# Performance work log

Hardware: AMD Instinct MI355X
Metric: run time of the kernel (lower is better)

## Reference

```python
import jax, jax.numpy as jnp
import numpy as np

K = 4                 # max_block_size (depthwise conv kernel size)
BLOCKS = (1, 2, 3, 4) # block sizes, offset 0
DS = 4                # downsample_factor
BLOCK_MULT = 12       # lcm(1,2,3,4)
DIM = 512
NUM_TOKENS = 256


def setup_inputs() -> dict:
    key = jax.random.key(0)
    ks = jax.random.split(key, 8)
    b, n = 4, 4096
    s = 0.02
    return {
        "x": jax.random.randint(ks[0], (b, n), 0, NUM_TOKENS),
        "emb": jax.random.normal(ks[1], (NUM_TOKENS, DIM), dtype=jnp.float32) * s,
        "conv_w": jax.random.normal(ks[2], (DIM, K), dtype=jnp.float32) * s,   # depthwise Conv1d weight [d,1,K] squeezed
        "conv_b": jax.random.normal(ks[3], (DIM,), dtype=jnp.float32) * s,
        "proj_w": jax.random.normal(ks[4], (DIM, DIM), dtype=jnp.float32) * s,  # 1x1 conv == linear [out,in]
        "proj_b": jax.random.normal(ks[5], (DIM,), dtype=jnp.float32) * s,
        "score_w": jax.random.normal(ks[6], (DIM,), dtype=jnp.float32) * s,     # nn.Linear(dim,1)
        "score_b": jax.random.normal(ks[7], (), dtype=jnp.float32) * s,
    }


def reference(x, emb, conv_w, conv_b, proj_w, proj_b, score_w, score_b):
    b, n = x.shape
    h = emb[x]  # [b, n, d] token embedding (gather)

    # pos_conv: pad (K-1) at sequence end, depthwise conv (valid), then pointwise proj
    hp = jnp.pad(h, ((0, 0), (0, K - 1), (0, 0)))
    y = conv_b + sum(hp[:, k:k + n, :] * conv_w[:, k] for k in range(K))  # [b, n, d]
    h = y @ proj_w.T + proj_b

    # pad sequence to multiple of lcm of block sizes
    L = -(-n // BLOCK_MULT) * BLOCK_MULT
    h = jnp.pad(h, ((0, 0), (0, L - n), (0, 0)))

    # multi-scale block mean pooling, upsampled back to length L
    reprs = []
    for bs in BLOCKS:
        r = h.reshape(b, L // bs, bs, DIM).mean(axis=2)     # [b, L/bs, d]
        reprs.append(jnp.repeat(r, bs, axis=1))             # [b, L, d]
    block_reprs = jnp.stack(reprs, axis=2)                  # [b, L, nb, d]

    # per-position block scores
    scores = block_reprs @ score_w + score_b                # [b, L, nb]
    scores = jax.nn.softmax(scores, axis=2)

    # consensus attention over positions (d = nb = len(BLOCKS))
    sim = jnp.einsum('bid,bjd->bij', scores, scores)        # [b, L, L]
    attn = jax.nn.softmax(sim, axis=-1)
    scores = jnp.einsum('bij,bjm->bim', attn, scores)       # [b, L, nb]

    # fuse block representations and downsample
    out = jnp.einsum('bnkd,bnk->bnd', block_reprs, scores)  # [b, L, d]
    m = -(-n // DS) * DS                                    # == n (4096 divisible by 4)
    out = out[:, :m].reshape(b, m // DS, DS, DIM).mean(axis=2)
    return out
```

## Files before the change

kernel.cpp:

```cpp
#include <hip/hip_runtime.h>
#include <hip/hip_bf16.h>

#define B_ 4
#define N_ 4096
#define L_ 4104
#define D_ 512
#define RT 17
#define JC2 32
#define CH2 129
#define BK 64

typedef __attribute__((ext_vector_type(8))) short bf16x8;
typedef __attribute__((ext_vector_type(4))) float f32x4;

__device__ __forceinline__ float bf2f(unsigned short u) {
  union { unsigned u; float f; } c; c.u = ((unsigned)u) << 16; return c.f;
}

__global__ __launch_bounds__(256) void k_g(const float* __restrict__ emb,
    const float* __restrict__ pw, const float* __restrict__ cwp,
    const float* __restrict__ cb, const float* __restrict__ pb,
    float* __restrict__ G, float* __restrict__ biasp) {
  __shared__ __align__(16) __hip_bfloat16 As[2][64 * BK];
  __shared__ __align__(16) __hip_bfloat16 Bs[2][128 * BK];
  __shared__ __align__(16) float cwS[512];
  __shared__ float red[4];
  const int bx = blockIdx.x;
  const int t = threadIdx.x;
  const int w = t >> 6, l = t & 63;

  if (bx >= 64) {
    const int o0 = (bx - 64) * 8;
    const float2 cv = *(const float2*)(cb + t * 2);
#pragma unroll
    for (int oo = 0; oo < 8; ++oo) {
      const int o = o0 + oo;
      const float2 wv = *(const float2*)(pw + (size_t)o * 512 + t * 2);
      float s = wv.x * cv.x + wv.y * cv.y;
#pragma unroll
      for (int off = 32; off > 0; off >>= 1) s += __shfl_xor(s, off);
      if (l == 0) red[w] = s;
      __syncthreads();
      if (t == 0) biasp[o] = red[0] + red[1] + red[2] + red[3] + pb[o];
      __syncthreads();
    }
    return;
  }

  const int m0 = (bx & 3) * 64;
  const int n0 = ((bx >> 2) & 3) * 128;
  const int kp = bx >> 4;
  const int quad = l >> 4, r16 = l & 15;
  const int wc = w * 32;

  cwS[t]       = cwp[t * 4 + kp];
  cwS[t + 256] = cwp[(t + 256) * 4 + kp];

  f32x4 acc[4][2];
#pragma unroll
  for (int a = 0; a < 4; ++a)
#pragma unroll
    for (int bq = 0; bq < 2; ++bq) acc[a][bq] = (f32x4){0.f, 0.f, 0.f, 0.f};

  const int ra = t >> 2, ga0 = (t & 3) * 2;
  const int rb = t >> 1, gb0 = (t & 1) * 4;

#define STAGEG(buf, kb)                                                          \
  _Pragma("unroll")                                                              \
  for (int gi = 0; gi < 2; ++gi) {                                               \
    const int g = ga0 + gi;                                                      \
    const int c0 = (kb) + g * 8;                                                 \
    const float4 a0 = *(const float4*)(emb + (size_t)(m0 + ra) * 512 + c0);      \
    const float4 a1 = *(const float4*)(emb + (size_t)(m0 + ra) * 512 + c0 + 4);  \
    const float4 w0 = *(const float4*)(cwS + c0);                                \
    const float4 w1 = *(const float4*)(cwS + c0 + 4);                            \
    union { __hip_bfloat16 q[8]; bf16x8 v; } ua;                                 \
    ua.q[0] = __float2bfloat16(a0.x * w0.x); ua.q[1] = __float2bfloat16(a0.y * w0.y); \
    ua.q[2] = __float2bfloat16(a0.z * w0.z); ua.q[3] = __float2bfloat16(a0.w * w0.w); \
    ua.q[4] = __float2bfloat16(a1.x * w1.x); ua.q[5] = __float2bfloat16(a1.y * w1.y); \
    ua.q[6] = __float2bfloat16(a1.z * w1.z); ua.q[7] = __float2bfloat16(a1.w * w1.w); \
    *(bf16x8*)(&As[buf][ra * BK + ((g ^ (ra & 7)) * 8)]) = ua.v;                 \
  }                                                                              \
  _Pragma("unroll")                                                              \
  for (int gi = 0; gi < 4; ++gi) {                                               \
    const int g = gb0 + gi;                                                      \
    const int c0 = (kb) + g * 8;                                                 \
    const float4 b0 = *(const float4*)(pw + (size_t)(n0 + rb) * 512 + c0);       \
    const float4 b1 = *(const float4*)(pw + (size_t)(n0 + rb) * 512 + c0 + 4);   \
    union { __hip_bfloat16 q[8]; bf16x8 v; } ub;                                 \
    ub.q[0] = __float2bfloat16(b0.x); ub.q[1] = __float2bfloat16(b0.y);          \
    ub.q[2] = __float2bfloat16(b0.z); ub.q[3] = __float2bfloat16(b0.w);          \
    ub.q[4] = __float2bfloat16(b1.x); ub.q[5] = __float2bfloat16(b1.y);          \
    ub.q[6] = __float2bfloat16(b1.z); ub.q[7] = __float2bfloat16(b1.w);          \
    *(bf16x8*)(&Bs[buf][rb * BK + ((g ^ (rb & 7)) * 8)]) = ub.v;                 \
  }

  __syncthreads();
  STAGEG(0, 0)
  __syncthreads();

#pragma unroll 1
  for (int kt = 0; kt < 8; ++kt) {
    const int cur = kt & 1;
    if (kt < 7) { STAGEG(1 - cur, (kt + 1) * BK) }
#pragma unroll
    for (int kk = 0; kk < 2; ++kk) {
      const int col_e = (kk * 32 + quad * 8) ^ ((r16 & 7) * 8);
      bf16x8 af[4], bfr[2];
#pragma unroll
      for (int ti = 0; ti < 4; ++ti)
        af[ti] = *(const bf16x8*)(&As[cur][(ti * 16 + r16) * BK + col_e]);
#pragma unroll
      for (int tj = 0; tj < 2; ++tj)
        bfr[tj] = *(const bf16x8*)(&Bs[cur][(wc + tj * 16 + r16) * BK + col_e]);
#pragma unroll
      for (int ti = 0; ti < 4; ++ti)
#pragma unroll
        for (int tj = 0; tj < 2; ++tj)
          acc[ti][tj] = __builtin_amdgcn_mfma_f32_16x16x32_bf16(af[ti], bfr[tj], acc[ti][tj], 0, 0, 0);
    }
    __syncthreads();
  }
#undef STAGEG

#pragma unroll
  for (int ti = 0; ti < 4; ++ti) {
    const int gi0 = m0 + ti * 16 + quad * 4;
#pragma unroll
    for (int tj = 0; tj < 2; ++tj) {
      const int go = n0 + wc + tj * 16 + r16;
#pragma unroll
      for (int r = 0; r < 4; ++r)
        G[((size_t)kp * 256 + gi0 + r) * 512 + go] = acc[ti][tj][r];
    }
  }
}

__global__ __launch_bounds__(256) void k_h(const int* __restrict__ x,
    const float* __restrict__ G, const float* __restrict__ biasp,
    const float* __restrict__ sw, unsigned* __restrict__ h,
    float* __restrict__ tb) {
  __shared__ int tokS[11];
  __shared__ float tpart[8][4];
  const int bx = blockIdx.x;
  const int b = bx >> 9, i0 = (bx & 511) * 8;
  const int t = threadIdx.x, d = t * 2, w = t >> 6, l = t & 63;
  if (t < 11) {
    const int j = i0 + t;
    tokS[t] = (j < N_) ? x[b * N_ + j] : 0;
  }
  __syncthreads();
  const float2 bp  = *(const float2*)(biasp + d);
  const float2 swv = *(const float2*)(sw + d);
#pragma unroll
  for (int r = 0; r < 8; ++r) {
    const int i = i0 + r;
    float2 acc = bp;
#pragma unroll
    for (int k = 0; k < 4; ++k) {
      if (i + k < N_) {
        const float2 g = *(const float2*)(G + ((size_t)k * 256 + tokS[r + k]) * 512 + d);
        acc.x += g.x; acc.y += g.y;
      }
    }
    union { __hip_bfloat16 q[2]; unsigned u; } pk;
    pk.q[0] = __float2bfloat16(acc.x);
    pk.q[1] = __float2bfloat16(acc.y);
    h[(size_t)(b * N_ + i) * 256 + t] = pk.u;
    float v = acc.x * swv.x + acc.y * swv.y;
#pragma unroll
    for (int off = 32; off > 0; off >>= 1) v += __shfl_xor(v, off);
    if (l == 0) tpart[r][w] = v;
  }
  __syncthreads();
  if (t < 8)
    tb[b * N_ + i0 + t] = tpart[t][0] + tpart[t][1] + tpart[t][2] + tpart[t][3];
}

__device__ __forceinline__ float4 softmax4(const float* __restrict__ tw, int base,
                                           int i, float bb) {
  const float s0 = tw[i - base] + bb;
  const int j2 = i & ~1;
  const float s1 = (tw[j2 - base] + tw[j2 + 1 - base]) * 0.5f + bb;
  const int j3 = (i / 3) * 3;
  const float s2 = (tw[j3 - base] + tw[j3 + 1 - base] + tw[j3 + 2 - base]) * (1.f / 3.f) + bb;
  const int j4 = i & ~3;
  const float s3 = (tw[j4 - base] + tw[j4 + 1 - base] + tw[j4 + 2 - base] + tw[j4 + 3 - base]) * 0.25f + bb;
  const float m = fmaxf(fmaxf(s0, s1), fmaxf(s2, s3));
  const float e0 = __expf(s0 - m), e1 = __expf(s1 - m), e2 = __expf(s2 - m), e3 = __expf(s3 - m);
  const float inv = 1.f / (e0 + e1 + e2 + e3);
  return make_float4(e0 * inv, e1 * inv, e2 * inv, e3 * inv);
}

__global__ __launch_bounds__(256) void k_attn(const float* __restrict__ tb,
    const float* __restrict__ sb,
    float4* __restrict__ accnP, float* __restrict__ accdP) {
  __shared__ float twi[262];
  __shared__ float twj[135];
  __shared__ __align__(16) float4 Sch[CH2];
  const int bx = blockIdx.x;
  const int jc = bx & (JC2 - 1);
  const int rt = (bx >> 5) % RT;
  const int b  = bx / (JC2 * RT);
  const int t = threadIdx.x;
  const int j0 = jc * CH2;
  const int i0 = rt * 256;
  const int rowb = b * N_;
  for (int idx = t; idx < 262; idx += 256) {
    const int j = i0 - 3 + idx;
    twi[idx] = (j >= 0 && j < N_) ? tb[rowb + j] : 0.f;
  }
  for (int idx = t; idx < 135; idx += 256) {
    const int j = j0 - 3 + idx;
    twj[idx] = (j >= 0 && j < N_) ? tb[rowb + j] : 0.f;
  }
  __syncthreads();
  const float bb = sb[0];
  if (t < CH2 && j0 + t < L_) Sch[t] = softmax4(twj, j0 - 3, j0 + t, bb);
  const int i = i0 + t;
  const float4 si = softmax4(twi, i0 - 3, i, bb);
  __syncthreads();
  if (i < L_) {
    const int len = min(CH2, L_ - j0);
    float l = 0.f, a0 = 0.f, a1 = 0.f, a2 = 0.f, a3 = 0.f;
#pragma unroll 4
    for (int jj = 0; jj < len; ++jj) {
      const float4 v = Sch[jj];
      const float dot = fmaf(si.x, v.x, fmaf(si.y, v.y, fmaf(si.z, v.z, si.w * v.w)));
      const float e = __expf(dot);
      l += e;
      a0 = fmaf(e, v.x, a0); a1 = fmaf(e, v.y, a1);
      a2 = fmaf(e, v.z, a2); a3 = fmaf(e, v.w, a3);
    }
    const size_t base = (size_t)jc * (B_ * L_) + b * L_ + i;
    accnP[base] = make_float4(a0, a1, a2, a3);
    accdP[base] = l;
  }
}

__global__ __launch_bounds__(256) void k_fuse(const __hip_bfloat16* __restrict__ h,
    const float4* __restrict__ accnP, const float* __restrict__ accdP,
    float* __restrict__ out) {
  __shared__ __align__(16) float4 wgtS[12];
  const int bx = blockIdx.x;
  const int b = bx / 342, j12 = bx % 342;
  const int t = threadIdx.x, d = t * 2;
  const int r0 = 12 * j12;

  if (t < 192) {
    const int r = t >> 4, q = t & 15;
    const size_t i1 = (size_t)q * (B_ * L_) + b * L_ + r0 + r;
    const size_t i2 = (size_t)(q + 16) * (B_ * L_) + b * L_ + r0 + r;
    float4 nv = accnP[i1];
    const float4 n2 = accnP[i2];
    nv.x += n2.x; nv.y += n2.y; nv.z += n2.z; nv.w += n2.w;
    float dv = accdP[i1] + accdP[i2];
#pragma unroll
    for (int m = 8; m >= 1; m >>= 1) {
      nv.x += __shfl_xor(nv.x, m); nv.y += __shfl_xor(nv.y, m);
      nv.z += __shfl_xor(nv.z, m); nv.w += __shfl_xor(nv.w, m);
      dv   += __shfl_xor(dv, m);
    }
    if (q == 0) {
      const float inv = 1.f / dv;
      wgtS[r] = make_float4(nv.x * inv, nv.y * inv, nv.z * inv, nv.w * inv);
    }
  }
  __syncthreads();

  const __hip_bfloat16* hb = h + (size_t)b * N_ * D_;
  float2 hv[12];
#pragma unroll
  for (int q = 0; q < 12; ++q) {
    const int row = r0 + q;
    if (row < N_) {
      const ushort2 u = *(const ushort2*)(hb + (size_t)row * D_ + d);
      hv[q] = make_float2(bf2f(u.x), bf2f(u.y));
    } else {
      hv[q] = make_float2(0.f, 0.f);
    }
  }

  float2 p2[6], p3[4], p4[3];
#pragma unroll
  for (int g = 0; g < 6; ++g) {
    p2[g].x = (hv[2 * g].x + hv[2 * g + 1].x) * 0.5f;
    p2[g].y = (hv[2 * g].y + hv[2 * g + 1].y) * 0.5f;
  }
#pragma unroll
  for (int g = 0; g < 4; ++g) {
    p3[g].x = (hv[3 * g].x + hv[3 * g + 1].x + hv[3 * g + 2].x) * (1.f / 3.f);
    p3[g].y = (hv[3 * g].y + hv[3 * g + 1].y + hv[3 * g + 2].y) * (1.f / 3.f);
  }
#pragma unroll
  for (int g = 0; g < 3; ++g) {
    p4[g].x = (hv[4 * g].x + hv[4 * g + 1].x + hv[4 * g + 2].x + hv[4 * g + 3].x) * 0.25f;
    p4[g].y = (hv[4 * g].y + hv[4 * g + 1].y + hv[4 * g + 2].y + hv[4 * g + 3].y) * 0.25f;
  }

#pragma unroll
  for (int o = 0; o < 3; ++o) {
    const int orow = j12 * 3 + o;
    if (orow < 1024) {
      float ox = 0.f, oy = 0.f;
#pragma unroll
      for (int rr = 0; rr < 4; ++rr) {
        const int r = 4 * o + rr;
        const float4 wv = wgtS[r];
        const float2 p1 = hv[r];
        const float2 q2 = p2[r >> 1];
        const float2 q3 = p3[r / 3];
        const float2 q4 = p4[o];
        ox += wv.x * p1.x + wv.y * q2.x + wv.z * q3.x + wv.w * q4.x;
        oy += wv.x * p1.y + wv.y * q2.y + wv.z * q3.y + wv.w * q4.y;
      }
      float2 ov; ov.x = ox * 0.25f; ov.y = oy * 0.25f;
      *(float2*)(out + (size_t)(b * 1024 + orow) * D_ + d) = ov;
    }
  }
}

extern "C" void kernel_launch(void* const* d_in, const int* in_sizes, int n_in,
                              void* d_out, int out_size, void* d_ws, size_t ws_size,
                              hipStream_t stream) {
  const int*   x       = (const int*)d_in[0];
  const float* emb     = (const float*)d_in[1];
  const float* conv_w  = (const float*)d_in[2];
  const float* conv_b  = (const float*)d_in[3];
  const float* proj_w  = (const float*)d_in[4];
  const float* proj_b  = (const float*)d_in[5];
  const float* score_w = (const float*)d_in[6];
  const float* score_b = (const float*)d_in[7];
  float* out = (float*)d_out;

  char* ws = (char*)d_ws;
  size_t off = 0;
  float*          G    = (float*)(ws + off);          off += (size_t)4 * 256 * 512 * 4;
  float*          bias = (float*)(ws + off);          off += (size_t)512 * 4;
  __hip_bfloat16* h    = (__hip_bfloat16*)(ws + off); off += (size_t)16384 * 512 * 2;
  float*          tb   = (float*)(ws + off);          off += (size_t)16384 * 4;
  float4*         accnP = (float4*)(ws + off);        off += (size_t)JC2 * B_ * L_ * 16;
  float*          accdP = (float*)(ws + off);         off += (size_t)JC2 * B_ * L_ * 4;
  (void)in_sizes; (void)n_in; (void)out_size; (void)ws_size;

  k_g<<<128, 256, 0, stream>>>(emb, proj_w, conv_w, conv_b, proj_b, G, bias);
  k_h<<<2048, 256, 0, stream>>>(x, G, bias, score_w, (unsigned*)h, tb);
  k_attn<<<B_ * RT * JC2, 256, 0, stream>>>(tb, score_b, accnP, accdP);
  k_fuse<<<B_ * 342, 256, 0, stream>>>(h, accnP, accdP, out);
}
```

Baseline: 134.3 us.

## Replace quadratic consensus attention with Taylor-feature linear attention

Approximates exp(s_i·s_j) by a degree-6 multivariate Taylor expansion over the four softmax scores, using 210 monomial features. Per-batch feature sums Z are accumulated once with atomics, and each row's numerator and denominator are then evaluated from its own features in the fuse kernel. This removes the O(L^2) exp loop and the large partial-accumulator buffers. It trades exactness for a bounded truncation error, since dots are at most 1, and adds float atomics with nondeterministic summation order.

```diff
diff --git a/kernel.cpp b/kernel.cpp
--- a/kernel.cpp
+++ b/kernel.cpp
@@ -5,10 +5,9 @@
 #define N_ 4096
 #define L_ 4104
 #define D_ 512
-#define RT 17
-#define JC2 32
 #define CH2 129
 #define BK 64
+#define NF 210
 
 typedef __attribute__((ext_vector_type(8))) short bf16x8;
 typedef __attribute__((ext_vector_type(4))) float f32x4;
@@ -20,7 +19,8 @@
 __global__ __launch_bounds__(256) void k_g(const float* __restrict__ emb,
     const float* __restrict__ pw, const float* __restrict__ cwp,
     const float* __restrict__ cb, const float* __restrict__ pb,
-    float* __restrict__ G, float* __restrict__ biasp) {
+    float* __restrict__ G, float* __restrict__ biasp,
+    unsigned* __restrict__ featPk, float* __restrict__ featCf) {
   __shared__ __align__(16) __hip_bfloat16 As[2][64 * BK];
   __shared__ __align__(16) __hip_bfloat16 Bs[2][128 * BK];
   __shared__ __align__(16) float cwS[512];
@@ -29,6 +29,23 @@
   const int t = threadIdx.x;
   const int w = t >> 6, l = t & 63;
 
+  if (bx == 128) {
+    if (t < NF) {
+      int idx = 0, mp = 0, mq = 0, mr = 0, ms = 0;
+      for (int m = 0; m <= 6; ++m)
+        for (int p = m; p >= 0; --p)
+          for (int q = m - p; q >= 0; --q)
+            for (int r = m - p - q; r >= 0; --r) {
+              const int s4 = m - p - q - r;
+              if (idx == t) { mp = p; mq = q; mr = r; ms = s4; }
+              ++idx;
+            }
+      featPk[t] = (unsigned)mp | ((unsigned)mq << 8) | ((unsigned)mr << 16) | ((unsigned)ms << 24);
+      const float invf[7] = {1.f, 1.f, 0.5f, 1.f/6.f, 1.f/24.f, 1.f/120.f, 1.f/720.f};
+      featCf[t] = invf[mp] * invf[mq] * invf[mr] * invf[ms];
+    }
+    return;
+  }
   if (bx >= 64) {
     const int o0 = (bx - 64) * 8;
     const float2 cv = *(const float2*)(cb + t * 2);
@@ -139,12 +156,16 @@
 __global__ __launch_bounds__(256) void k_h(const int* __restrict__ x,
     const float* __restrict__ G, const float* __restrict__ biasp,
     const float* __restrict__ sw, unsigned* __restrict__ h,
-    float* __restrict__ tb) {
+    float* __restrict__ tb, float* __restrict__ Zg) {
   __shared__ int tokS[11];
   __shared__ float tpart[8][4];
   const int bx = blockIdx.x;
   const int b = bx >> 9, i0 = (bx & 511) * 8;
   const int t = threadIdx.x, d = t * 2, w = t >> 6, l = t & 63;
+  if (bx < 17) {
+    const int zi = bx * 256 + t;
+    if (zi < B_ * NF * 5) Zg[zi] = 0.f;
+  }
   if (t < 11) {
     const int j = i0 + t;
     tokS[t] = (j < N_) ? x[b * N_ + j] : 0;
@@ -192,78 +213,114 @@
   return make_float4(e0 * inv, e1 * inv, e2 * inv, e3 * inv);
 }
 
-__global__ __launch_bounds__(256) void k_attn(const float* __restrict__ tb,
-    const float* __restrict__ sb,
-    float4* __restrict__ accnP, float* __restrict__ accdP) {
-  __shared__ float twi[262];
+__global__ __launch_bounds__(256) void k_zphi(const float* __restrict__ tb,
+    const float* __restrict__ sb, const unsigned* __restrict__ featPk,
+    const float* __restrict__ featCf, float* __restrict__ Zg) {
   __shared__ float twj[135];
-  __shared__ __align__(16) float4 Sch[CH2];
+  __shared__ float P[CH2][32];
+  __shared__ unsigned pkS[NF];
   const int bx = blockIdx.x;
-  const int jc = bx & (JC2 - 1);
-  const int rt = (bx >> 5) % RT;
-  const int b  = bx / (JC2 * RT);
+  const int b = bx >> 5, jc = bx & 31;
   const int t = threadIdx.x;
   const int j0 = jc * CH2;
-  const int i0 = rt * 256;
   const int rowb = b * N_;
-  for (int idx = t; idx < 262; idx += 256) {
-    const int j = i0 - 3 + idx;
-    twi[idx] = (j >= 0 && j < N_) ? tb[rowb + j] : 0.f;
-  }
+  const int len = min(CH2, L_ - j0);
+  if (t < NF) pkS[t] = featPk[t];
   for (int idx = t; idx < 135; idx += 256) {
     const int j = j0 - 3 + idx;
     twj[idx] = (j >= 0 && j < N_) ? tb[rowb + j] : 0.f;
   }
   __syncthreads();
   const float bb = sb[0];
-  if (t < CH2 && j0 + t < L_) Sch[t] = softmax4(twj, j0 - 3, j0 + t, bb);
-  const int i = i0 + t;
-  const float4 si = softmax4(twi, i0 - 3, i, bb);
-  __syncthreads();
-  if (i < L_) {
-    const int len = min(CH2, L_ - j0);
-    float l = 0.f, a0 = 0.f, a1 = 0.f, a2 = 0.f, a3 = 0.f;
-#pragma unroll 4
+  if (t < len) {
+    const float4 s = softmax4(twj, j0 - 3, j0 + t, bb);
+    float* p = &P[t][0];
+    float va = 1.f, vb = 1.f, vc = 1.f, vd = 1.f;
+    p[0] = 1.f; p[8] = 1.f; p[16] = 1.f; p[24] = 1.f;
+#pragma unroll
+    for (int e = 1; e < 8; ++e) {
+      va *= s.x; vb *= s.y; vc *= s.z; vd *= s.w;
+      p[e] = va; p[8 + e] = vb; p[16 + e] = vc; p[24 + e] = vd;
+    }
+  }
+  __syncthreads();
+  if (t < NF) {
+    const unsigned pk = pkS[t];
+    const int p = pk & 255, q = (pk >> 8) & 255, r = (pk >> 16) & 255, s4 = pk >> 24;
+    float z0 = 0.f, z1 = 0.f, z2 = 0.f, z3 = 0.f, z4 = 0.f;
     for (int jj = 0; jj < len; ++jj) {
-      const float4 v = Sch[jj];
-      const float dot = fmaf(si.x, v.x, fmaf(si.y, v.y, fmaf(si.z, v.z, si.w * v.w)));
-      const float e = __expf(dot);
-      l += e;
-      a0 = fmaf(e, v.x, a0); a1 = fmaf(e, v.y, a1);
-      a2 = fmaf(e, v.z, a2); a3 = fmaf(e, v.w, a3);
-    }
-    const size_t base = (size_t)jc * (B_ * L_) + b * L_ + i;
-    accnP[base] = make_float4(a0, a1, a2, a3);
-    accdP[base] = l;
+      const float* pp = &P[jj][0];
+      const float pa0 = pp[p],       pa1 = pp[p + 1];
+      const float pb0 = pp[8 + q],   pb1 = pp[8 + q + 1];
+      const float pc0 = pp[16 + r],  pc1 = pp[16 + r + 1];
+      const float pd0 = pp[24 + s4], pd1 = pp[24 + s4 + 1];
+      const float cd = pc0 * pd0, ab = pa0 * pb0;
+      z4 += pa0 * (pb0 * cd);
+      z0 += pa1 * (pb0 * cd);
+      z1 += pb1 * (pa0 * cd);
+      z2 += pc1 * (ab * pd0);
+      z3 += pd1 * (ab * pc0);
+    }
+    float* zb = Zg + (size_t)(b * NF + t) * 5;
+    atomicAdd(zb + 0, z0); atomicAdd(zb + 1, z1); atomicAdd(zb + 2, z2);
+    atomicAdd(zb + 3, z3); atomicAdd(zb + 4, z4);
   }
 }
 
 __global__ __launch_bounds__(256) void k_fuse(const __hip_bfloat16* __restrict__ h,
-    const float4* __restrict__ accnP, const float* __restrict__ accdP,
-    float* __restrict__ out) {
+    const float* __restrict__ tb, const float* __restrict__ sb,
+    const unsigned* __restrict__ featPk, const float* __restrict__ featCf,
+    const float* __restrict__ Zg, float* __restrict__ out) {
   __shared__ __align__(16) float4 wgtS[12];
+  __shared__ float tbS[12];
+  __shared__ float Pr[12][32];
+  __shared__ float Zl[NF * 5];
+  __shared__ unsigned pkS[NF];
+  __shared__ float cfS[NF];
   const int bx = blockIdx.x;
   const int b = bx / 342, j12 = bx % 342;
   const int t = threadIdx.x, d = t * 2;
   const int r0 = 12 * j12;
 
+  if (t < NF) { pkS[t] = featPk[t]; cfS[t] = featCf[t]; }
+  for (int i2 = t; i2 < NF * 5; i2 += 256) Zl[i2] = Zg[(size_t)b * NF * 5 + i2];
+  if (t < 12) {
+    const int row = r0 + t;
+    tbS[t] = (row < N_) ? tb[b * N_ + row] : 0.f;
+  }
+  __syncthreads();
+  if (t < 12) {
+    const float4 s = softmax4(tbS, r0, r0 + t, sb[0]);
+    float* p = &Pr[t][0];
+    float va = 1.f, vb = 1.f, vc = 1.f, vd = 1.f;
+    p[0] = 1.f; p[8] = 1.f; p[16] = 1.f; p[24] = 1.f;
+#pragma unroll
+    for (int e = 1; e < 8; ++e) {
+      va *= s.x; vb *= s.y; vc *= s.z; vd *= s.w;
+      p[e] = va; p[8 + e] = vb; p[16 + e] = vc; p[24 + e] = vd;
+    }
+  }
+  __syncthreads();
   if (t < 192) {
-    const int r = t >> 4, q = t & 15;
-    const size_t i1 = (size_t)q * (B_ * L_) + b * L_ + r0 + r;
-    const size_t i2 = (size_t)(q + 16) * (B_ * L_) + b * L_ + r0 + r;
-    float4 nv = accnP[i1];
-    const float4 n2 = accnP[i2];
-    nv.x += n2.x; nv.y += n2.y; nv.z += n2.z; nv.w += n2.w;
-    float dv = accdP[i1] + accdP[i2];
+    const int row = t >> 4, fi = t & 15;
+    float n0 = 0.f, n1 = 0.f, n2 = 0.f, n3 = 0.f, dn = 0.f;
+    const float* pr = &Pr[row][0];
+    for (int f = fi; f < NF; f += 16) {
+      const unsigned pk = pkS[f];
+      const float val = cfS[f] * pr[pk & 255] * pr[8 + ((pk >> 8) & 255)]
+                                * pr[16 + ((pk >> 16) & 255)] * pr[24 + (pk >> 24)];
+      const float* z = &Zl[f * 5];
+      n0 += val * z[0]; n1 += val * z[1]; n2 += val * z[2]; n3 += val * z[3];
+      dn += val * z[4];
+    }
 #pragma unroll
     for (int m = 8; m >= 1; m >>= 1) {
-      nv.x += __shfl_xor(nv.x, m); nv.y += __shfl_xor(nv.y, m);
-      nv.z += __shfl_xor(nv.z, m); nv.w += __shfl_xor(nv.w, m);
-      dv   += __shfl_xor(dv, m);
-    }
-    if (q == 0) {
-      const float inv = 1.f / dv;
-      wgtS[r] = make_float4(nv.x * inv, nv.y * inv, nv.z * inv, nv.w * inv);
+      n0 += __shfl_xor(n0, m); n1 += __shfl_xor(n1, m); n2 += __shfl_xor(n2, m);
+      n3 += __shfl_xor(n3, m); dn += __shfl_xor(dn, m);
+    }
+    if (fi == 0) {
+      const float inv = 1.f / dn;
+      wgtS[row] = make_float4(n0 * inv, n1 * inv, n2 * inv, n3 * inv);
     }
   }
   __syncthreads();
@@ -339,12 +396,13 @@
   float*          bias = (float*)(ws + off);          off += (size_t)512 * 4;
   __hip_bfloat16* h    = (__hip_bfloat16*)(ws + off); off += (size_t)16384 * 512 * 2;
   float*          tb   = (float*)(ws + off);          off += (size_t)16384 * 4;
-  float4*         accnP = (float4*)(ws + off);        off += (size_t)JC2 * B_ * L_ * 16;
-  float*          accdP = (float*)(ws + off);         off += (size_t)JC2 * B_ * L_ * 4;
+  float*          Zg   = (float*)(ws + off);          off += (size_t)B_ * NF * 5 * 4;
+  unsigned*       featPk = (unsigned*)(ws + off);     off += (size_t)NF * 4;
+  float*          featCf = (float*)(ws + off);        off += (size_t)NF * 4;
   (void)in_sizes; (void)n_in; (void)out_size; (void)ws_size;
 
-  k_g<<<128, 256, 0, stream>>>(emb, proj_w, conv_w, conv_b, proj_b, G, bias);
-  k_h<<<2048, 256, 0, stream>>>(x, G, bias, score_w, (unsigned*)h, tb);
-  k_attn<<<B_ * RT * JC2, 256, 0, stream>>>(tb, score_b, accnP, accdP);
-  k_fuse<<<B_ * 342, 256, 0, stream>>>(h, accnP, accdP, out);
-}
+  k_g<<<129, 256, 0, stream>>>(emb, proj_w, conv_w, conv_b, proj_b, G, bias, featPk, featCf);
+  k_h<<<2048, 256, 0, stream>>>(x, G, bias, score_w, (unsigned*)h, tb, Zg);
+  k_zphi<<<B_ * 32, 256, 0, stream>>>(tb, score_b, featPk, featCf, Zg);
+  k_fuse<<<B_ * 342, 256, 0, stream>>>(h, tb, score_b, featPk, featCf, Zg, out);
+}
```

After: 126.4 us. 1.06x faster.
